# Kernel optimization log

Hardware: AMD Instinct MI355X
Metric: run time of the kernel (lower is better)

Reference implementation:

```python
import jax, jax.numpy as jnp
import numpy as np

NUM_LAYERS = 5
EMB = 300
N_GRAPHS = 4096
BN_EPS = 1e-5
TEMP = 0.04


def _gnn_encode(x, edge_index, edge_attr, atom_emb1, atom_emb2,
                edge_emb1, edge_emb2, mlp_w1, mlp_b1, mlp_w2, mlp_b2,
                bn_gamma, bn_beta):
    n = x.shape[0]
    h = atom_emb1[x[:, 0]] + atom_emb2[x[:, 1]]  # [N, EMB]
    src, dst = edge_index[0], edge_index[1]
    for l in range(NUM_LAYERS):
        eemb = edge_emb1[l][edge_attr[:, 0]] + edge_emb2[l][edge_attr[:, 1]]  # [E, EMB]
        self_emb = edge_emb1[l][4] + edge_emb2[l][0]  # self-loop edge_attr = [4, 0]
        agg = jax.ops.segment_sum(h[src] + eemb, dst, num_segments=n)
        agg = agg + h + self_emb  # self-loop messages
        h = jax.nn.relu(agg @ mlp_w1[l] + mlp_b1[l]) @ mlp_w2[l] + mlp_b2[l]
        mean = jnp.mean(h, axis=0)
        var = jnp.var(h, axis=0)
        h = (h - mean) / jnp.sqrt(var + BN_EPS) * bn_gamma[l] + bn_beta[l]
        if l != NUM_LAYERS - 1:
            h = jax.nn.relu(h)
    return h


def _branch(x, edge_index, edge_attr, node_batch, params):
    h = _gnn_encode(x, edge_index, edge_attr, *params[:-2])
    h = h @ params[-2] + params[-1]  # projector
    s = jax.ops.segment_sum(h, node_batch, num_segments=N_GRAPHS)
    cnt = jax.ops.segment_sum(jnp.ones((h.shape[0],), h.dtype), node_batch,
                              num_segments=N_GRAPHS)
    g = s / jnp.maximum(cnt, 1.0)[:, None]  # global mean pool
    norm = jnp.maximum(jnp.linalg.norm(g, axis=1, keepdims=True), 1e-12)
    return g / norm


def setup_inputs() -> dict:
    key = jax.random.key(0)
    ks = jax.random.split(key, 24)
    f = jnp.float32
    inp = {}
    inp['x0'] = jax.random.randint(ks[0], (100000, 2), 0, 3)
    inp['edge_index0'] = jax.random.randint(ks[1], (2, 400000), 0, 100000)
    inp['edge_attr0'] = jax.random.randint(ks[2], (400000, 2), 0, 3)
    inp['batch0'] = jnp.sort(jax.random.randint(ks[3], (100000,), 0, N_GRAPHS))
    inp['x1'] = jax.random.randint(ks[4], (100000, 2), 0, 3)
    inp['edge_index1'] = jax.random.randint(ks[5], (2, 400000), 0, 100000)
    inp['edge_attr1'] = jax.random.randint(ks[6], (400000, 2), 0, 3)
    inp['batch1'] = jnp.sort(jax.random.randint(ks[7], (100000,), 0, N_GRAPHS))
    s = 0.02
    inp['atom_emb1'] = jax.random.normal(ks[8], (120, EMB), f) * s
    inp['atom_emb2'] = jax.random.normal(ks[9], (3, EMB), f) * s
    inp['edge_emb1'] = jax.random.normal(ks[10], (NUM_LAYERS, 6, EMB), f) * s
    inp['edge_emb2'] = jax.random.normal(ks[11], (NUM_LAYERS, 3, EMB), f) * s
    inp['mlp_w1'] = jax.random.normal(ks[12], (NUM_LAYERS, EMB, 2 * EMB), f) * s
    inp['mlp_b1'] = jnp.zeros((NUM_LAYERS, 2 * EMB), f)
    inp['mlp_w2'] = jax.random.normal(ks[13], (NUM_LAYERS, 2 * EMB, EMB), f) * s
    inp['mlp_b2'] = jnp.zeros((NUM_LAYERS, EMB), f)
    inp['bn_gamma'] = jnp.ones((NUM_LAYERS, EMB), f)
    inp['bn_beta'] = jnp.zeros((NUM_LAYERS, EMB), f)
    inp['proj_w'] = jax.random.normal(ks[14], (EMB, EMB), f) * s
    inp['proj_b'] = jnp.zeros((EMB,), f)
    return inp


def reference(x0, edge_index0, edge_attr0, batch0,
              x1, edge_index1, edge_attr1, batch1,
              atom_emb1, atom_emb2, edge_emb1, edge_emb2,
              mlp_w1, mlp_b1, mlp_w2, mlp_b2, bn_gamma, bn_beta,
              proj_w, proj_b):
    params = (atom_emb1, atom_emb2, edge_emb1, edge_emb2,
              mlp_w1, mlp_b1, mlp_w2, mlp_b2, bn_gamma, bn_beta,
              proj_w, proj_b)
    f0 = _branch(x0, edge_index0, edge_attr0, batch0, params)
    f1 = _branch(x1, edge_index1, edge_attr1, batch1, params)
    logits = (f0 @ f1.T) / TEMP  # [G, G]
    return logits
```

## Files before the change

### kernel.cpp

```cpp
#include <hip/hip_runtime.h>
#include <hip/hip_bf16.h>


#define EMB 300
#define EMBC 75
#define AGGP 320
#define AGGC 80
#define HID 600
#define NGRAPH 4096
#define BN_EPS 1e-5f
#define INV_TEMP 25.0f
#define NRED 24

typedef __hip_bfloat16 bf16;
struct __align__(8) bf4 { bf16 x, y, z, w; };
typedef __attribute__((ext_vector_type(8))) short short8;
typedef __attribute__((ext_vector_type(4))) float float4v;

__device__ inline float b2f(bf16 v) { return __bfloat162float(v); }
__device__ inline bf16 f2b(float v) { return __float2bfloat16(v); }
__device__ inline unsigned short f2bu(float f) {
    bf16 b = __float2bfloat16(f); unsigned short u; __builtin_memcpy(&u, &b, 2); return u;
}

typedef const unsigned int __attribute__((address_space(1)))* gas_t;
typedef unsigned int __attribute__((address_space(3)))* las_t;
__device__ __forceinline__ void gl_lds16(const unsigned short* g, unsigned short* l) {
    __builtin_amdgcn_global_load_lds((gas_t)g, (las_t)l, 16, 0, 0);
}


__global__ void k_zero_f(float* __restrict__ p, int n) {
    int i = blockIdx.x * blockDim.x + threadIdx.x;
    if (i < n) p[i] = 0.f;
}
__global__ void k_zero_i(int* __restrict__ p, int n) {
    int i = blockIdx.x * blockDim.x + threadIdx.x;
    if (i < n) p[i] = 0;
}


__global__ void k_split(const float* __restrict__ W, int K, int N, int Kpad, int Npad,
                        unsigned short* __restrict__ hi, unsigned short* __restrict__ lo) {
    int idx = blockIdx.x * blockDim.x + threadIdx.x;
    if (idx >= Npad * Kpad) return;
    int n = idx / Kpad, k = idx % Kpad;
    float v = (n < N && k < K) ? W[(size_t)k * N + n] : 0.f;
    bf16 h = __float2bfloat16(v);
    float rem = v - __bfloat162float(h);
    bf16 l = __float2bfloat16(rem);
    unsigned short hu, lu;
    __builtin_memcpy(&hu, &h, 2); __builtin_memcpy(&lu, &l, 2);
    hi[idx] = hu; lo[idx] = lu;
}

__global__ void k_fsplit(const float* __restrict__ f, unsigned short* __restrict__ hi,
                         unsigned short* __restrict__ lo, int G) {
    int idx = blockIdx.x * blockDim.x + threadIdx.x;
    if (idx >= G * AGGP) return;
    int g = idx / AGGP, c = idx % AGGP;
    float v = (c < EMB) ? f[(size_t)g * EMB + c] : 0.f;
    bf16 h = __float2bfloat16(v);
    float rem = v - __bfloat162float(h);
    unsigned short hu; __builtin_memcpy(&hu, &h, 2);
    hi[idx] = hu;
    lo[idx] = f2bu(rem);
}


__global__ void k_hist(const int* __restrict__ ei, int* __restrict__ deg, int E) {
    int e = blockIdx.x * blockDim.x + threadIdx.x;
    if (e < E) atomicAdd(&deg[ei[E + e]], 1);
}

__global__ void k_chunksum(const int* __restrict__ deg, int* __restrict__ csum, int total) {
    __shared__ int s[256];
    int t = threadIdx.x, i = blockIdx.x * 256 + t;
    s[t] = (i < total) ? deg[i] : 0;
    __syncthreads();
    for (int off = 128; off > 0; off >>= 1) {
        if (t < off) s[t] += s[t + off];
        __syncthreads();
    }
    if (t == 0) csum[blockIdx.x] = s[0];
}

__global__ void k_scanchunks(const int* __restrict__ csum, int* __restrict__ coff, int n) {
    if (threadIdx.x == 0) {
        int acc = 0;
        for (int b = 0; b < n; ++b) { coff[b] = acc; acc += csum[b]; }
    }
}

__global__ void k_scan2(const int* __restrict__ deg, const int* __restrict__ coff,
                        int* __restrict__ rowstart, int total) {
    __shared__ int s[256];
    int t = threadIdx.x, b = blockIdx.x, i = b * 256 + t;
    int v = (i < total) ? deg[i] : 0;
    s[t] = v;
    __syncthreads();
    for (int off = 1; off < 256; off <<= 1) {
        int u = (t >= off) ? s[t - off] : 0;
        __syncthreads();
        s[t] += u;
        __syncthreads();
    }
    if (i < total) rowstart[i] = coff[b] + s[t] - v;
}

__global__ void k_initcursor(const int* __restrict__ rowstart, int* __restrict__ cur, int N) {
    int i = blockIdx.x * blockDim.x + threadIdx.x;
    if (i < N) cur[i] = rowstart[i];
}

__global__ void k_fill(const int* __restrict__ ei, int* __restrict__ cur,
                       int* __restrict__ esorted, int E) {
    int e = blockIdx.x * blockDim.x + threadIdx.x;
    if (e < E) {
        int p = atomicAdd(&cur[ei[E + e]], 1);
        esorted[p] = e;
    }
}

__global__ void k_pack(const int* __restrict__ ei, const int* __restrict__ ea,
                       const int* __restrict__ esorted, int* __restrict__ packed, int E) {
    int p = blockIdx.x * blockDim.x + threadIdx.x;
    if (p >= E) return;
    int e = esorted[p];
    int s = ei[e];
    int cb = ea[2 * e] * 3 + ea[2 * e + 1];
    packed[p] = s | (cb << 17);
}

__global__ void k_sortb(const int* __restrict__ rowstart, int* __restrict__ packed, int N) {
    int n = blockIdx.x * blockDim.x + threadIdx.x;
    if (n >= N) return;
    int p0 = rowstart[n], p1 = rowstart[n + 1];
    for (int i = p0 + 1; i < p1; ++i) {
        int v = packed[i];
        int j = i - 1;
        while (j >= p0 && packed[j] > v) { packed[j + 1] = packed[j]; --j; }
        packed[j + 1] = v;
    }
}

__global__ void k_gstart(const int* __restrict__ batch, int* __restrict__ gstart, int N) {
    int g = blockIdx.x * blockDim.x + threadIdx.x;
    if (g > NGRAPH) return;
    int lo = 0, hi = N;
    while (lo < hi) { int mid = (lo + hi) >> 1; if (batch[mid] < g) lo = mid + 1; else hi = mid; }
    gstart[g] = lo;
}

__global__ void k_combo(const float4* __restrict__ e1, const float4* __restrict__ e2,
                        float4* __restrict__ cmb) {
    int t = blockIdx.x * blockDim.x + threadIdx.x;
    if (t >= 18 * EMBC) return;
    int cb = t / EMBC, j = t % EMBC;
    float4 u = e1[(cb / 3) * EMBC + j];
    float4 v = e2[(cb % 3) * EMBC + j];
    float4 r; r.x = u.x + v.x; r.y = u.y + v.y; r.z = u.z + v.z; r.w = u.w + v.w;
    cmb[t] = r;
}


__global__ void k_init_h(const int* __restrict__ x,
                         const float4* __restrict__ ae1,
                         const float4* __restrict__ ae2,
                         bf4* __restrict__ h4, int N) {
    int idx = blockIdx.x * blockDim.x + threadIdx.x;
    if (idx >= N * EMBC) return;
    int i = idx / EMBC, j = idx % EMBC;
    int a0 = x[2 * i], a1 = x[2 * i + 1];
    float4 u = ae1[a0 * EMBC + j];
    float4 v = ae2[a1 * EMBC + j];
    bf4 r = { f2b(u.x + v.x), f2b(u.y + v.y), f2b(u.z + v.z), f2b(u.w + v.w) };
    h4[idx] = r;
}

__global__ void k_aggregate(const bf4* __restrict__ h4,
                            const int* __restrict__ packed,
                            const float4* __restrict__ cmb,
                            const int* __restrict__ rowstart,
                            const float* __restrict__ stats, int use_aff,
                            bf4* __restrict__ agg4, int N) {
    int idx = blockIdx.x * blockDim.x + threadIdx.x;
    if (idx >= N * AGGC) return;
    int n = idx / AGGC, j = idx % AGGC;
    if (j >= EMBC) {
        bf4 z = { f2b(0.f), f2b(0.f), f2b(0.f), f2b(0.f) };
        agg4[idx] = z;
        return;
    }
    float4 sc = make_float4(1.f, 1.f, 1.f, 1.f);
    float4 sh = make_float4(0.f, 0.f, 0.f, 0.f);
    if (use_aff) {
        sc = ((const float4*)stats)[j];
        sh = ((const float4*)(stats + EMB))[j];
    }
    bf4 hv = h4[(size_t)n * EMBC + j];
    float hx = b2f(hv.x), hy = b2f(hv.y), hz = b2f(hv.z), hw = b2f(hv.w);
    if (use_aff) {
        hx = fmaxf(hx * sc.x + sh.x, 0.f); hy = fmaxf(hy * sc.y + sh.y, 0.f);
        hz = fmaxf(hz * sc.z + sh.z, 0.f); hw = fmaxf(hw * sc.w + sh.w, 0.f);
    }
    float4 s0 = cmb[12 * EMBC + j];
    float ax = hx + s0.x, ay = hy + s0.y, az = hz + s0.z, aw = hw + s0.w;
    int p0 = rowstart[n], p1 = rowstart[n + 1];
    for (int p = p0; p < p1; ++p) {
        int u = packed[p];
        int s = u & 131071;
        int cb = u >> 17;
        bf4 hs = h4[(size_t)s * EMBC + j];
        float gx = b2f(hs.x), gy = b2f(hs.y), gz = b2f(hs.z), gw = b2f(hs.w);
        if (use_aff) {
            gx = fmaxf(gx * sc.x + sh.x, 0.f); gy = fmaxf(gy * sc.y + sh.y, 0.f);
            gz = fmaxf(gz * sc.z + sh.z, 0.f); gw = fmaxf(gw * sc.w + sh.w, 0.f);
        }
        float4 cv = cmb[cb * EMBC + j];
        ax += gx + cv.x; ay += gy + cv.y;
        az += gz + cv.z; aw += gw + cv.w;
    }
    bf4 r = { f2b(ax), f2b(ay), f2b(az), f2b(aw) };
    agg4[idx] = r;
}

__global__ void k_bncopy(const bf4* __restrict__ h4, const float* __restrict__ stats,
                         bf4* __restrict__ dst, int N) {
    int idx = blockIdx.x * blockDim.x + threadIdx.x;
    if (idx >= N * AGGC) return;
    int n = idx / AGGC, j = idx % AGGC;
    if (j >= EMBC) {
        bf4 z = { f2b(0.f), f2b(0.f), f2b(0.f), f2b(0.f) };
        dst[idx] = z;
        return;
    }
    float4 sc = ((const float4*)stats)[j];
    float4 sh = ((const float4*)(stats + EMB))[j];
    bf4 v = h4[(size_t)n * EMBC + j];
    bf4 r = { f2b(b2f(v.x) * sc.x + sh.x), f2b(b2f(v.y) * sc.y + sh.y),
              f2b(b2f(v.z) * sc.z + sh.z), f2b(b2f(v.w) * sc.w + sh.w) };
    dst[idx] = r;
}


#define GBM 128
#define GBN 128
#define GBK 64

__global__ __launch_bounds__(256)
void k_gemm_mfma(const unsigned short* __restrict__ A, int lda, int Kpad,
                 const unsigned short* __restrict__ Bhi,
                 const unsigned short* __restrict__ Blo, int ldb,
                 const float* __restrict__ bias,
                 unsigned short* __restrict__ C, int ldc, int M, int Nc, int relu,
                 float* __restrict__ psum, int do_stats) {
    __shared__ unsigned short As[GBM][GBK];
    __shared__ unsigned short Bh[GBN][GBK];
    __shared__ unsigned short Bl[GBN][GBK];

    int tid = threadIdx.x;
    int wv = tid >> 6, lane = tid & 63;
    int quad = lane >> 4, l16 = lane & 15;
    int wm = wv & 1, wn = wv >> 1;
    int lrow = lane >> 3;
    int gchunk = (lane & 7) ^ lrow;
    int sw = lane & 7;

    int ncols = gridDim.x, nrows = gridDim.y;
    int lin = blockIdx.y * ncols + blockIdx.x;
    int g = lin / (8 * ncols);
    int rem = lin - g * 8 * ncols;
    int rows_in = min(8, nrows - g * 8);
    int colb = rem / rows_in;
    int rowb = g * 8 + (rem - colb * rows_in);
    int row0 = rowb * GBM;
    int col0 = colb * GBN;

    float4v acc[4][4];
    #pragma unroll
    for (int i = 0; i < 4; ++i)
        #pragma unroll
        for (int j = 0; j < 4; ++j) acc[i][j] = (float4v){0.f, 0.f, 0.f, 0.f};

    for (int k0 = 0; k0 < Kpad; k0 += GBK) {
        #pragma unroll
        for (int j = 0; j < 4; ++j) {
            int r = 32 * wv + 8 * j + lrow;
            int gr = min(row0 + r, M - 1);
            gl_lds16(A + (size_t)gr * lda + k0 + gchunk * 8, &As[32 * wv + 8 * j][0]);
        }
        #pragma unroll
        for (int j = 0; j < 4; ++j) {
            int r = 32 * wv + 8 * j + lrow;
            size_t go = (size_t)(col0 + r) * ldb + k0 + gchunk * 8;
            gl_lds16(Bhi + go, &Bh[32 * wv + 8 * j][0]);
            gl_lds16(Blo + go, &Bl[32 * wv + 8 * j][0]);
        }
        __syncthreads();

        int mbase = wm * 64, nbase = wn * 64;
        #pragma unroll
        for (int ks = 0; ks < GBK; ks += 32) {
            int pc = ((ks >> 3) + quad) ^ sw;
            short8 a[4];
            #pragma unroll
            for (int mt = 0; mt < 4; ++mt)
                a[mt] = *(const short8*)(&As[mbase + mt * 16 + l16][pc * 8]);
            #pragma unroll
            for (int nt = 0; nt < 4; ++nt) {
                short8 bh = *(const short8*)(&Bh[nbase + nt * 16 + l16][pc * 8]);
                short8 bl = *(const short8*)(&Bl[nbase + nt * 16 + l16][pc * 8]);
                #pragma unroll
                for (int mt = 0; mt < 4; ++mt) {
                    acc[mt][nt] = __builtin_amdgcn_mfma_f32_16x16x32_bf16(a[mt], bh, acc[mt][nt], 0, 0, 0);
                    acc[mt][nt] = __builtin_amdgcn_mfma_f32_16x16x32_bf16(a[mt], bl, acc[mt][nt], 0, 0, 0);
                }
            }
        }
        __syncthreads();
    }

    float sv[4], qv[4];
    #pragma unroll
    for (int nt = 0; nt < 4; ++nt) { sv[nt] = 0.f; qv[nt] = 0.f; }
    #pragma unroll
    for (int mt = 0; mt < 4; ++mt) {
        int rbase = row0 + wm * 64 + mt * 16 + quad * 4;
        #pragma unroll
        for (int nt = 0; nt < 4; ++nt) {
            int c = col0 + wn * 64 + nt * 16 + l16;
            if (c >= Nc) continue;
            float bs = bias[c];
            #pragma unroll
            for (int i = 0; i < 4; ++i) {
                int r = rbase + i;
                if (r >= M) continue;
                float v = acc[mt][nt][i] + bs;
                if (relu) v = fmaxf(v, 0.f);
                if (do_stats) { sv[nt] += v; qv[nt] += v * v; }
                C[(size_t)r * ldc + c] = f2bu(v);
            }
        }
    }
    if (do_stats) {
        float* cred = (float*)(&As[0][0]);
        #pragma unroll
        for (int nt = 0; nt < 4; ++nt) {
            float s = sv[nt], q = qv[nt];
            s += __shfl_down(s, 32, 64); s += __shfl_down(s, 16, 64);
            q += __shfl_down(q, 32, 64); q += __shfl_down(q, 16, 64);
            if (quad == 0) {
                cred[wv * 128 + nt * 16 + l16] = s;
                cred[wv * 128 + 64 + nt * 16 + l16] = q;
            }
        }
        __syncthreads();
        if (tid < 128) {
            int c = col0 + tid;
            int cin = tid & 63, wvn = tid >> 6;
            float s = cred[(wvn * 2 + 0) * 128 + cin] + cred[(wvn * 2 + 1) * 128 + cin];
            float q = cred[(wvn * 2 + 0) * 128 + 64 + cin] + cred[(wvn * 2 + 1) * 128 + 64 + cin];
            psum[(size_t)rowb * 768 + c] = s;
            psum[(size_t)rowb * 768 + 384 + c] = q;
        }
    }
}


__global__ __launch_bounds__(256)
void k_logits(const unsigned short* __restrict__ Ahg, const unsigned short* __restrict__ Alg,
              const unsigned short* __restrict__ Bhg, const unsigned short* __restrict__ Blg,
              float* __restrict__ C, float scale) {
    __shared__ unsigned short sAh[64][64];
    __shared__ unsigned short sAl[64][64];
    __shared__ unsigned short sBh[128][64];
    __shared__ unsigned short sBl[128][64];

    int tid = threadIdx.x;
    int wv = tid >> 6, lane = tid & 63;
    int quad = lane >> 4, l16 = lane & 15;
    int lrow = lane >> 3;
    int gchunk = (lane & 7) ^ lrow;
    int sw = lane & 7;
    int row0 = blockIdx.y * 64;
    int col0 = blockIdx.x * 128;

    float4v acc[8];
    #pragma unroll
    for (int j = 0; j < 8; ++j) acc[j] = (float4v){0.f, 0.f, 0.f, 0.f};

    for (int k0 = 0; k0 < AGGP; k0 += 64) {
        #pragma unroll
        for (int j = 0; j < 2; ++j) {
            int r = 16 * wv + 8 * j + lrow;
            size_t go = (size_t)(row0 + r) * AGGP + k0 + gchunk * 8;
            gl_lds16(Ahg + go, &sAh[16 * wv + 8 * j][0]);
            gl_lds16(Alg + go, &sAl[16 * wv + 8 * j][0]);
        }
        #pragma unroll
        for (int j = 0; j < 4; ++j) {
            int r = 32 * wv + 8 * j + lrow;
            size_t go = (size_t)(col0 + r) * AGGP + k0 + gchunk * 8;
            gl_lds16(Bhg + go, &sBh[32 * wv + 8 * j][0]);
            gl_lds16(Blg + go, &sBl[32 * wv + 8 * j][0]);
        }
        __syncthreads();

        #pragma unroll
        for (int ks = 0; ks < 64; ks += 32) {
            int pc = ((ks >> 3) + quad) ^ sw;
            short8 ah = *(const short8*)(&sAh[wv * 16 + l16][pc * 8]);
            short8 al = *(const short8*)(&sAl[wv * 16 + l16][pc * 8]);
            #pragma unroll
            for (int nt = 0; nt < 8; ++nt) {
                short8 bh = *(const short8*)(&sBh[nt * 16 + l16][pc * 8]);
                short8 bl = *(const short8*)(&sBl[nt * 16 + l16][pc * 8]);
                acc[nt] = __builtin_amdgcn_mfma_f32_16x16x32_bf16(ah, bh, acc[nt], 0, 0, 0);
                acc[nt] = __builtin_amdgcn_mfma_f32_16x16x32_bf16(ah, bl, acc[nt], 0, 0, 0);
                acc[nt] = __builtin_amdgcn_mfma_f32_16x16x32_bf16(al, bh, acc[nt], 0, 0, 0);
            }
        }
        __syncthreads();
    }

    int rbase = row0 + wv * 16 + quad * 4;
    #pragma unroll
    for (int nt = 0; nt < 8; ++nt) {
        int c = col0 + nt * 16 + l16;
        #pragma unroll
        for (int i = 0; i < 4; ++i)
            C[(size_t)(rbase + i) * NGRAPH + c] = acc[nt][i] * scale;
    }
}


__global__ void k_statred(const float* __restrict__ psum, float* __restrict__ part2, int nrb) {
    int b = blockIdx.x, c = threadIdx.x;
    float acc = 0.f;
    for (int r = b; r < nrb; r += NRED) acc += psum[(size_t)r * 768 + c];
    part2[b * 768 + c] = acc;
}

__global__ void k_bn_prep(const float* __restrict__ part2, float* __restrict__ stats,
                          const float* __restrict__ gamma, const float* __restrict__ beta,
                          float invN) {
    int c = threadIdx.x;
    if (c >= EMB) return;
    float s = 0.f, q = 0.f;
    for (int b = 0; b < NRED; ++b) {
        s += part2[b * 768 + c];
        q += part2[b * 768 + 384 + c];
    }
    float mean = s * invN;
    float var = q * invN - mean * mean;
    float scale = gamma[c] * rsqrtf(var + BN_EPS);
    stats[c] = scale;
    stats[EMB + c] = beta[c] - mean * scale;
}


__global__ void k_poolnorm(const bf16* __restrict__ proj, const int* __restrict__ gstart,
                           float* __restrict__ f) {
    int g = blockIdx.x, t = threadIdx.x;
    int s = gstart[g], e = gstart[g + 1];
    float sum = 0.f;
    if (t < EMB)
        for (int r = s; r < e; ++r) sum += b2f(proj[(size_t)r * AGGP + t]);
    float cnt = fmaxf((float)(e - s), 1.f);
    float m = sum / cnt;
    float q = (t < EMB) ? m * m : 0.f;
    for (int off = 32; off > 0; off >>= 1) q += __shfl_down(q, off, 64);
    __shared__ float red[5];
    int lane = t & 63, wid = t >> 6;
    if (lane == 0) red[wid] = q;
    __syncthreads();
    float tot = red[0] + red[1] + red[2] + red[3] + red[4];
    float invn = 1.f / fmaxf(sqrtf(tot), 1e-12f);
    if (t < EMB) f[(size_t)g * EMB + t] = m * invn;
}


static inline int ceil_div(int a, int b) { return (a + b - 1) / b; }

extern "C" void kernel_launch(void* const* d_in, const int* in_sizes, int n_in,
                              void* d_out, int out_size, void* d_ws, size_t ws_size,
                              hipStream_t stream) {
    const int N = in_sizes[0] / 2;
    const int E = in_sizes[1] / 2;

    const int* x[2]  = { (const int*)d_in[0], (const int*)d_in[4] };
    const int* ei[2] = { (const int*)d_in[1], (const int*)d_in[5] };
    const int* ea[2] = { (const int*)d_in[2], (const int*)d_in[6] };
    const int* bt[2] = { (const int*)d_in[3], (const int*)d_in[7] };
    const float* atom1 = (const float*)d_in[8];
    const float* atom2 = (const float*)d_in[9];
    const float* ee1 = (const float*)d_in[10];
    const float* ee2 = (const float*)d_in[11];
    const float* w1  = (const float*)d_in[12];
    const float* b1  = (const float*)d_in[13];
    const float* w2  = (const float*)d_in[14];
    const float* b2  = (const float*)d_in[15];
    const float* gam = (const float*)d_in[16];
    const float* bet = (const float*)d_in[17];
    const float* pw  = (const float*)d_in[18];
    const float* pb  = (const float*)d_in[19];
    float* out = (float*)d_out;

    char* wsb = (char*)d_ws;
    bf16* h    = (bf16*)(wsb);
    bf16* agg  = (bf16*)(wsb + 60000000);
    bf16* hid  = (bf16*)(wsb + 124000000);
    float* guard = (float*)(wsb + 244000000);
    float* f0  = (float*)(wsb + 244000256);
    float* f1  = (float*)(wsb + 248915456);
    unsigned short* f0hi = (unsigned short*)(wsb + 124000000);
    unsigned short* f0lo = (unsigned short*)(wsb + 126621440);
    unsigned short* f1hi = (unsigned short*)(wsb + 129242880);
    unsigned short* f1lo = (unsigned short*)(wsb + 131864320);

    int* deg      = (int*)d_out;
    int* rowstart = deg + (N + 1);
    int* cursor   = rowstart + (N + 1);
    int* esorted  = cursor + N;
    int* packed   = esorted + E;
    int* csum     = packed + E;
    int* coff     = csum + 512;
    int* gstart   = coff + 512;
    float* stats  = (float*)(gstart + 4097);
    float* cmb    = stats + 600;
    char* splits  = (char*)d_out + 4500224;
    unsigned short* w1hi = (unsigned short*)(splits);
    unsigned short* w1lo = (unsigned short*)(splits + 2048000);
    unsigned short* w2hi = (unsigned short*)(splits + 4096000);
    unsigned short* w2lo = (unsigned short*)(splits + 6553600);
    unsigned short* pjhi = (unsigned short*)(splits + 9011200);
    unsigned short* pjlo = (unsigned short*)(splits + 9256960);
    float* psum  = (float*)((char*)d_out + 20971520);
    float* part2 = (float*)((char*)d_out + 25165824);

    const int TB = 256;
    const int nh_blocks = ceil_div(N * EMBC, TB);
    const int na_blocks = ceil_div(N * AGGC, TB);
    const int nchunks = ceil_div(N + 1, 256);
    const float invN = 1.f / (float)N;

    k_zero_f<<<1, 64, 0, stream>>>(guard, 64);

    for (int l = 0; l < 5; ++l) {
        k_split<<<ceil_div(640 * 320, TB), TB, 0, stream>>>(
            w1 + (size_t)l * EMB * HID, EMB, HID, 320, 640,
            w1hi + (size_t)l * 640 * 320, w1lo + (size_t)l * 640 * 320);
        k_split<<<ceil_div(384 * 640, TB), TB, 0, stream>>>(
            w2 + (size_t)l * HID * EMB, HID, EMB, 640, 384,
            w2hi + (size_t)l * 384 * 640, w2lo + (size_t)l * 384 * 640);
    }
    k_split<<<ceil_div(384 * 320, TB), TB, 0, stream>>>(pw, EMB, EMB, 320, 384, pjhi, pjlo);

    const int mrows = ceil_div(N, GBM);
    dim3 g1(5, mrows);
    dim3 g2(3, mrows);
    dim3 glg(32, 64);

    for (int br = 0; br < 2; ++br) {
        float* fout = br == 0 ? f0 : f1;
        k_zero_i<<<ceil_div(N + 1, TB), TB, 0, stream>>>(deg, N + 1);
        k_hist<<<ceil_div(E, TB), TB, 0, stream>>>(ei[br], deg, E);
        k_chunksum<<<nchunks, 256, 0, stream>>>(deg, csum, N + 1);
        k_scanchunks<<<1, 64, 0, stream>>>(csum, coff, nchunks);
        k_scan2<<<nchunks, 256, 0, stream>>>(deg, coff, rowstart, N + 1);
        k_initcursor<<<ceil_div(N, TB), TB, 0, stream>>>(rowstart, cursor, N);
        k_fill<<<ceil_div(E, TB), TB, 0, stream>>>(ei[br], cursor, esorted, E);
        k_pack<<<ceil_div(E, TB), TB, 0, stream>>>(ei[br], ea[br], esorted, packed, E);
        k_sortb<<<ceil_div(N, TB), TB, 0, stream>>>(rowstart, packed, N);
        k_gstart<<<ceil_div(NGRAPH + 1, TB), TB, 0, stream>>>(bt[br], gstart, N);
        k_init_h<<<nh_blocks, TB, 0, stream>>>(x[br], (const float4*)atom1,
                                               (const float4*)atom2, (bf4*)h, N);
        for (int l = 0; l < 5; ++l) {
            k_combo<<<ceil_div(18 * EMBC, TB), TB, 0, stream>>>(
                (const float4*)(ee1 + (size_t)l * 6 * EMB),
                (const float4*)(ee2 + (size_t)l * 3 * EMB), (float4*)cmb);
            k_aggregate<<<na_blocks, TB, 0, stream>>>((const bf4*)h, packed,
                                                      (const float4*)cmb, rowstart,
                                                      stats, l > 0, (bf4*)agg, N);
            k_gemm_mfma<<<g1, 256, 0, stream>>>(
                (const unsigned short*)agg, AGGP, AGGP,
                w1hi + (size_t)l * 640 * 320, w1lo + (size_t)l * 640 * 320, 320,
                b1 + (size_t)l * HID, (unsigned short*)hid, HID, N, HID, 1,
                nullptr, 0);
            k_gemm_mfma<<<g2, 256, 0, stream>>>(
                (const unsigned short*)hid, HID, 640,
                w2hi + (size_t)l * 384 * 640, w2lo + (size_t)l * 384 * 640, 640,
                b2 + (size_t)l * EMB, (unsigned short*)h, EMB, N, EMB, 0,
                psum, 1);
            k_statred<<<NRED, 768, 0, stream>>>(psum, part2, mrows);
            k_bn_prep<<<1, 320, 0, stream>>>(part2, stats, gam + (size_t)l * EMB,
                                             bet + (size_t)l * EMB, invN);
        }
        k_bncopy<<<na_blocks, TB, 0, stream>>>((const bf4*)h, stats, (bf4*)hid, N);
        k_gemm_mfma<<<g2, 256, 0, stream>>>(
            (const unsigned short*)hid, AGGP, AGGP,
            pjhi, pjlo, 320, pb, (unsigned short*)agg, AGGP, N, EMB, 0,
            nullptr, 0);
        k_poolnorm<<<NGRAPH, 320, 0, stream>>>(agg, gstart, fout);
    }
    k_fsplit<<<ceil_div(NGRAPH * AGGP, TB), TB, 0, stream>>>(f0, f0hi, f0lo, NGRAPH);
    k_fsplit<<<ceil_div(NGRAPH * AGGP, TB), TB, 0, stream>>>(f1, f1hi, f1lo, NGRAPH);
    k_logits<<<glg, 256, 0, stream>>>(f0hi, f0lo, f1hi, f1lo, out, INV_TEMP);
}
```

Baseline: 5.007 ms.

## Double-buffer GEMM LDS tiles with smaller K step to overlap loads

The MFMA GEMM now uses two LDS buffers with a K tile of 32, issuing the global-to-LDS loads for the next tile before computing on the current one. This removes the wait between loading and computing that the single-buffer loop had on every K iteration. The swizzle and the per-thread source pointers are recomputed for the narrower tile. In exchange there are twice as many iterations and barriers, and each barrier covers less math.

```diff
diff --git a/kernel.cpp b/kernel.cpp
--- a/kernel.cpp
+++ b/kernel.cpp
@@ -246,7 +246,7 @@
 
 #define GBM 128
 #define GBN 128
-#define GBK 64
+#define GBK 32
 
 __global__ __launch_bounds__(256)
 void k_gemm_mfma(const unsigned short* __restrict__ A, int lda, int Kpad,
@@ -255,17 +255,18 @@
                  const float* __restrict__ bias,
                  unsigned short* __restrict__ C, int ldc, int M, int Nc, int relu,
                  float* __restrict__ psum, int do_stats) {
-    __shared__ unsigned short As[GBM][GBK];
-    __shared__ unsigned short Bh[GBN][GBK];
-    __shared__ unsigned short Bl[GBN][GBK];
+    __shared__ unsigned short As[2][GBM][GBK];
+    __shared__ unsigned short Bh[2][GBN][GBK];
+    __shared__ unsigned short Bl[2][GBN][GBK];
 
     int tid = threadIdx.x;
     int wv = tid >> 6, lane = tid & 63;
     int quad = lane >> 4, l16 = lane & 15;
     int wm = wv & 1, wn = wv >> 1;
-    int lrow = lane >> 3;
-    int gchunk = (lane & 7) ^ lrow;
-    int sw = lane & 7;
+
+    int srow = lane >> 2;
+    int gch = (lane & 3) ^ ((lane >> 3) & 3);
+    int pc = quad ^ ((l16 >> 1) & 3);
 
     int ncols = gridDim.x, nrows = gridDim.y;
     int lin = blockIdx.y * ncols + blockIdx.x;
@@ -277,45 +278,55 @@
     int row0 = rowb * GBM;
     int col0 = colb * GBN;
 
+    const unsigned short* Asrc[2];
+    const unsigned short* Bsrc[2];
+    #pragma unroll
+    for (int j = 0; j < 2; ++j) {
+        int r = 32 * wv + 16 * j + srow;
+        Asrc[j] = A + (size_t)min(row0 + r, M - 1) * lda + gch * 8;
+        Bsrc[j] = Bhi + (size_t)(col0 + r) * ldb + gch * 8;
+    }
+    const size_t dBL = (size_t)(Blo - Bhi);
+
     float4v acc[4][4];
     #pragma unroll
     for (int i = 0; i < 4; ++i)
         #pragma unroll
         for (int j = 0; j < 4; ++j) acc[i][j] = (float4v){0.f, 0.f, 0.f, 0.f};
 
-    for (int k0 = 0; k0 < Kpad; k0 += GBK) {
-        #pragma unroll
-        for (int j = 0; j < 4; ++j) {
-            int r = 32 * wv + 8 * j + lrow;
-            int gr = min(row0 + r, M - 1);
-            gl_lds16(A + (size_t)gr * lda + k0 + gchunk * 8, &As[32 * wv + 8 * j][0]);
-        }
-        #pragma unroll
-        for (int j = 0; j < 4; ++j) {
-            int r = 32 * wv + 8 * j + lrow;
-            size_t go = (size_t)(col0 + r) * ldb + k0 + gchunk * 8;
-            gl_lds16(Bhi + go, &Bh[32 * wv + 8 * j][0]);
-            gl_lds16(Blo + go, &Bl[32 * wv + 8 * j][0]);
-        }
-        __syncthreads();
-
-        int mbase = wm * 64, nbase = wn * 64;
-        #pragma unroll
-        for (int ks = 0; ks < GBK; ks += 32) {
-            int pc = ((ks >> 3) + quad) ^ sw;
-            short8 a[4];
+    const int nt = Kpad / GBK;
+
+    #pragma unroll
+    for (int j = 0; j < 2; ++j) {
+        gl_lds16(Asrc[j], &As[0][32 * wv + 16 * j][0]);
+        gl_lds16(Bsrc[j], &Bh[0][32 * wv + 16 * j][0]);
+        gl_lds16(Bsrc[j] + dBL, &Bl[0][32 * wv + 16 * j][0]);
+    }
+    __syncthreads();
+
+    for (int t = 0; t < nt; ++t) {
+        int cur = t & 1;
+        if (t + 1 < nt) {
+            int k1 = (t + 1) * GBK;
             #pragma unroll
-            for (int mt = 0; mt < 4; ++mt)
-                a[mt] = *(const short8*)(&As[mbase + mt * 16 + l16][pc * 8]);
+            for (int j = 0; j < 2; ++j) {
+                gl_lds16(Asrc[j] + k1, &As[cur ^ 1][32 * wv + 16 * j][0]);
+                gl_lds16(Bsrc[j] + k1, &Bh[cur ^ 1][32 * wv + 16 * j][0]);
+                gl_lds16(Bsrc[j] + k1 + dBL, &Bl[cur ^ 1][32 * wv + 16 * j][0]);
+            }
+        }
+        short8 a[4];
+        #pragma unroll
+        for (int mt = 0; mt < 4; ++mt)
+            a[mt] = *(const short8*)(&As[cur][wm * 64 + mt * 16 + l16][pc * 8]);
+        #pragma unroll
+        for (int ntl = 0; ntl < 4; ++ntl) {
+            short8 bh = *(const short8*)(&Bh[cur][wn * 64 + ntl * 16 + l16][pc * 8]);
+            short8 bl = *(const short8*)(&Bl[cur][wn * 64 + ntl * 16 + l16][pc * 8]);
             #pragma unroll
-            for (int nt = 0; nt < 4; ++nt) {
-                short8 bh = *(const short8*)(&Bh[nbase + nt * 16 + l16][pc * 8]);
-                short8 bl = *(const short8*)(&Bl[nbase + nt * 16 + l16][pc * 8]);
-                #pragma unroll
-                for (int mt = 0; mt < 4; ++mt) {
-                    acc[mt][nt] = __builtin_amdgcn_mfma_f32_16x16x32_bf16(a[mt], bh, acc[mt][nt], 0, 0, 0);
-                    acc[mt][nt] = __builtin_amdgcn_mfma_f32_16x16x32_bf16(a[mt], bl, acc[mt][nt], 0, 0, 0);
-                }
+            for (int mt = 0; mt < 4; ++mt) {
+                acc[mt][ntl] = __builtin_amdgcn_mfma_f32_16x16x32_bf16(a[mt], bh, acc[mt][ntl], 0, 0, 0);
+                acc[mt][ntl] = __builtin_amdgcn_mfma_f32_16x16x32_bf16(a[mt], bl, acc[mt][ntl], 0, 0, 0);
             }
         }
         __syncthreads();
@@ -323,36 +334,36 @@
 
     float sv[4], qv[4];
     #pragma unroll
-    for (int nt = 0; nt < 4; ++nt) { sv[nt] = 0.f; qv[nt] = 0.f; }
+    for (int ntl = 0; ntl < 4; ++ntl) { sv[ntl] = 0.f; qv[ntl] = 0.f; }
     #pragma unroll
     for (int mt = 0; mt < 4; ++mt) {
         int rbase = row0 + wm * 64 + mt * 16 + quad * 4;
         #pragma unroll
-        for (int nt = 0; nt < 4; ++nt) {
-            int c = col0 + wn * 64 + nt * 16 + l16;
+        for (int ntl = 0; ntl < 4; ++ntl) {
+            int c = col0 + wn * 64 + ntl * 16 + l16;
             if (c >= Nc) continue;
             float bs = bias[c];
             #pragma unroll
             for (int i = 0; i < 4; ++i) {
                 int r = rbase + i;
                 if (r >= M) continue;
-                float v = acc[mt][nt][i] + bs;
+                float v = acc[mt][ntl][i] + bs;
                 if (relu) v = fmaxf(v, 0.f);
-                if (do_stats) { sv[nt] += v; qv[nt] += v * v; }
+                if (do_stats) { sv[ntl] += v; qv[ntl] += v * v; }
                 C[(size_t)r * ldc + c] = f2bu(v);
             }
         }
     }
     if (do_stats) {
-        float* cred = (float*)(&As[0][0]);
-        #pragma unroll
-        for (int nt = 0; nt < 4; ++nt) {
-            float s = sv[nt], q = qv[nt];
+        float* cred = (float*)(&As[0][0][0]);
+        #pragma unroll
+        for (int ntl = 0; ntl < 4; ++ntl) {
+            float s = sv[ntl], q = qv[ntl];
             s += __shfl_down(s, 32, 64); s += __shfl_down(s, 16, 64);
             q += __shfl_down(q, 32, 64); q += __shfl_down(q, 16, 64);
             if (quad == 0) {
-                cred[wv * 128 + nt * 16 + l16] = s;
-                cred[wv * 128 + 64 + nt * 16 + l16] = q;
+                cred[wv * 128 + ntl * 16 + l16] = s;
+                cred[wv * 128 + 64 + ntl * 16 + l16] = q;
             }
         }
         __syncthreads();
```

Result: faster. 4.663 ms (-6.9%).
